# Optimization experiments

Hardware: AMD Instinct MI355X
Metric: run time of the kernel (lower is better)

## Reference

```python
import jax, jax.numpy as jnp
import numpy as np

NUM_HEADS = 16
HEAD_DIM = 64
INNER = NUM_HEADS * HEAD_DIM  # 1024
QUERY_DIM = 1024
CONTEXT_DIM = 768
SCALE = HEAD_DIM ** -0.5


def setup_inputs() -> dict:
    key = jax.random.key(0)
    ks = jax.random.split(key, 6)
    B, NQ, NKV = 8, 1024, 2048
    query = jax.random.normal(ks[0], (B, NQ, QUERY_DIM), dtype=jnp.float32)
    context = jax.random.normal(ks[1], (B, NKV, CONTEXT_DIM), dtype=jnp.float32)
    # weights stored as [in, out] (transpose of torch Linear), math-equivalent
    w_q = jax.random.normal(ks[2], (QUERY_DIM, INNER), dtype=jnp.float32) * (QUERY_DIM ** -0.5)
    w_kv = jax.random.normal(ks[3], (CONTEXT_DIM, 2 * INNER), dtype=jnp.float32) * (CONTEXT_DIM ** -0.5)
    w_out = jax.random.normal(ks[4], (INNER, QUERY_DIM), dtype=jnp.float32) * (INNER ** -0.5)
    b_out = jax.random.normal(ks[5], (QUERY_DIM,), dtype=jnp.float32) * 0.01
    return {"query": query, "context": context, "w_q": w_q, "w_kv": w_kv,
            "w_out": w_out, "b_out": b_out}


def reference(query, context, w_q, w_kv, w_out, b_out):
    B, NQ, _ = query.shape
    NKV = context.shape[1]
    q = query @ w_q                              # [B, NQ, INNER]
    kv = context @ w_kv                          # [B, NKV, 2*INNER]
    k, v = jnp.split(kv, 2, axis=-1)
    # reshape to [B, H, N, D]
    q = q.reshape(B, NQ, NUM_HEADS, HEAD_DIM).transpose(0, 2, 1, 3)
    k = k.reshape(B, NKV, NUM_HEADS, HEAD_DIM).transpose(0, 2, 1, 3)
    v = v.reshape(B, NKV, NUM_HEADS, HEAD_DIM).transpose(0, 2, 1, 3)
    scores = jnp.einsum('bhqd,bhkd->bhqk', q, k) * SCALE
    attn = jax.nn.softmax(scores, axis=-1)
    out = jnp.einsum('bhqk,bhkd->bhqd', attn, v)  # [B, H, NQ, D]
    out = out.transpose(0, 2, 1, 3).reshape(B, NQ, INNER)
    return out @ w_out + b_out
```

## Files before the change

kernel.cpp:

```cpp
#include <hip/hip_runtime.h>
#include <stdint.h>

typedef __bf16 bf16_t;
typedef bf16_t bf16x8 __attribute__((ext_vector_type(8)));
typedef float f32x4 __attribute__((ext_vector_type(4)));
typedef float f32x16 __attribute__((ext_vector_type(16)));

__device__ __forceinline__ unsigned short f2bf(float x) {
    unsigned u = __builtin_bit_cast(unsigned, x);
    u = (u + 0x7FFFu + ((u >> 16) & 1u)) >> 16;
    return (unsigned short)u;
}

__device__ __forceinline__ unsigned pk_bf16(float lo, float hi) {
    unsigned u0 = __builtin_bit_cast(unsigned, lo) + 0x8000u;
    unsigned u1 = __builtin_bit_cast(unsigned, hi) + 0x8000u;
    return __builtin_amdgcn_perm(u1, u0, 0x07060302u);
}

__device__ __forceinline__ void async_load16(const void* g, void* lds) {
    auto* gp = reinterpret_cast<const __attribute__((address_space(1))) uint32_t*>(
        reinterpret_cast<uintptr_t>(g));
    auto* lp = reinterpret_cast<__attribute__((address_space(3))) uint32_t*>(
        reinterpret_cast<uintptr_t>(lds));
    __builtin_amdgcn_global_load_lds(gp, lp, 16, 0, 0);
}

__global__ __launch_bounds__(256) void cast_f32_bf16(const float* __restrict__ src,
                                                     unsigned short* __restrict__ dst,
                                                     int n8) {
    int i = blockIdx.x * 256 + threadIdx.x;
    if (i >= n8) return;
    const float4* s4 = (const float4*)src;
    float4 a = s4[i * 2], b = s4[i * 2 + 1];
    uint4 o;
    o.x = (unsigned)f2bf(a.x) | ((unsigned)f2bf(a.y) << 16);
    o.y = (unsigned)f2bf(a.z) | ((unsigned)f2bf(a.w) << 16);
    o.z = (unsigned)f2bf(b.x) | ((unsigned)f2bf(b.y) << 16);
    o.w = (unsigned)f2bf(b.z) | ((unsigned)f2bf(b.w) << 16);
    ((uint4*)dst)[i] = o;
}

__global__ __launch_bounds__(256) void transcast(const float* __restrict__ src,
                                                 unsigned short* __restrict__ dst,
                                                 int K, int N, float scale) {
    __shared__ float tile[32][33];
    int x = threadIdx.x, y = threadIdx.y;
    int c0 = blockIdx.x * 32, r0 = blockIdx.y * 32;
    #pragma unroll
    for (int i = 0; i < 32; i += 8)
        tile[y + i][x] = src[(size_t)(r0 + y + i) * N + c0 + x];
    __syncthreads();
    #pragma unroll
    for (int i = 0; i < 32; i += 8)
        dst[(size_t)(c0 + y + i) * K + r0 + x] = f2bf(tile[x][y + i] * scale);
}

template <int EPI>
__global__ __launch_bounds__(256) void gemm_bt(const unsigned short* __restrict__ A,
                                               const unsigned short* __restrict__ Bt,
                                               void* __restrict__ Cout,
                                               const float* __restrict__ bias,
                                               int K, int N, int nkt) {
    __shared__ __align__(16) unsigned short lA[128 * 64];
    __shared__ __align__(16) unsigned short lB[128 * 64];
    const int tid = threadIdx.x;
    const int w = tid >> 6, l = tid & 63;
    const int wm = w >> 1, wn = w & 1;
    const int row0 = blockIdx.y * 128, col0 = blockIdx.x * 128;
    const int lrow = l & 15, lq = l >> 4;
    const int srow = l >> 3;
    const int scol = ((l & 7) ^ srow) * 8;

    f32x4 acc[4][4];
    #pragma unroll
    for (int i = 0; i < 4; ++i)
        #pragma unroll
        for (int j = 0; j < 4; ++j) acc[i][j] = (f32x4)0.f;

    for (int kt = 0; kt < nkt; ++kt) {
        const int k0 = kt * 64;
        __syncthreads();
        #pragma unroll
        for (int q = 0; q < 4; ++q) {
            int r = (w * 4 + q) * 8 + srow;
            async_load16(A + (size_t)(row0 + r) * K + k0 + scol,
                         (char*)lA + (w * 4 + q) * 1024);
            async_load16(Bt + (size_t)(col0 + r) * K + k0 + scol,
                         (char*)lB + (w * 4 + q) * 1024);
        }
        __syncthreads();
        #pragma unroll
        for (int kc = 0; kc < 2; ++kc) {
            const int pc = ((kc * 4 + lq) ^ (lrow & 7)) * 16;
            bf16x8 af[4], bfr[4];
            #pragma unroll
            for (int i = 0; i < 4; ++i)
                af[i] = *(const bf16x8*)((const char*)lA + (wm * 64 + i * 16 + lrow) * 128 + pc);
            #pragma unroll
            for (int j = 0; j < 4; ++j)
                bfr[j] = *(const bf16x8*)((const char*)lB + (wn * 64 + j * 16 + lrow) * 128 + pc);
            #pragma unroll
            for (int i = 0; i < 4; ++i)
                #pragma unroll
                for (int j = 0; j < 4; ++j)
                    acc[i][j] = __builtin_amdgcn_mfma_f32_16x16x32_bf16(af[i], bfr[j],
                                                                        acc[i][j], 0, 0, 0);
        }
    }
    #pragma unroll
    for (int i = 0; i < 4; ++i) {
        const int grow0 = row0 + wm * 64 + i * 16 + lq * 4;
        #pragma unroll
        for (int j = 0; j < 4; ++j) {
            const int gcol = col0 + wn * 64 + j * 16 + lrow;
            #pragma unroll
            for (int r = 0; r < 4; ++r) {
                float v = acc[i][j][r];
                int grow = grow0 + r;
                if (EPI == 0) {
                    ((unsigned short*)Cout)[(size_t)grow * N + gcol] = f2bf(v);
                } else {
                    ((float*)Cout)[(size_t)grow * N + gcol] = v + bias[gcol];
                }
            }
        }
    }
}

__global__ __launch_bounds__(256, 2) void gemm_kv(const unsigned short* __restrict__ A,
                                                  const unsigned short* __restrict__ Bt,
                                                  unsigned short* __restrict__ Kb,
                                                  unsigned short* __restrict__ Vt) {
    __shared__ __align__(16) unsigned short lA[256 * 64];
    __shared__ __align__(16) unsigned short lB[128 * 64];
    const int tid = threadIdx.x;
    const int w = tid >> 6, l = tid & 63;
    const int wm = w >> 1, wn = w & 1;
    const int row0 = blockIdx.y * 256, col0 = blockIdx.x * 128;
    const int r32 = l & 31, hw = l >> 5;
    const int srow = l >> 3, scol = ((l & 7) ^ srow) * 8;

    f32x16 acc[4][2];
    #pragma unroll
    for (int mi = 0; mi < 4; ++mi)
        #pragma unroll
        for (int ni = 0; ni < 2; ++ni) acc[mi][ni] = (f32x16)0.f;

    const unsigned short* ga = A + (size_t)(row0 + w * 8 + srow) * 768 + scol;
    const unsigned short* gb = Bt + (size_t)(col0 + w * 8 + srow) * 768 + scol;
    char* lAw = (char*)lA + (w * 8) * 128;
    char* lBw = (char*)lB + (w * 8) * 128;
    const char* lap = (const char*)lA + (wm * 128 + r32) * 128;
    const char* lbp = (const char*)lB + (wn * 64 + r32) * 128;
    const int r7 = r32 & 7;

    for (int kt = 0; kt < 12; ++kt) {
        __syncthreads();
        #pragma unroll
        for (int q = 0; q < 8; ++q)
            async_load16(ga + (size_t)q * 32 * 768, lAw + q * 32 * 128);
        #pragma unroll
        for (int q = 0; q < 4; ++q)
            async_load16(gb + (size_t)q * 32 * 768, lBw + q * 32 * 128);
        ga += 64;
        gb += 64;
        __syncthreads();
        #pragma unroll
        for (int ks = 0; ks < 4; ++ks) {
            const int off = ((ks * 2 + hw) ^ r7) * 16;
            bf16x8 af[4], bfr[2];
            #pragma unroll
            for (int mi = 0; mi < 4; ++mi)
                af[mi] = *(const bf16x8*)(lap + mi * 32 * 128 + off);
            #pragma unroll
            for (int ni = 0; ni < 2; ++ni)
                bfr[ni] = *(const bf16x8*)(lbp + ni * 32 * 128 + off);
            #pragma unroll
            for (int mi = 0; mi < 4; ++mi)
                #pragma unroll
                for (int ni = 0; ni < 2; ++ni)
                    acc[mi][ni] = __builtin_amdgcn_mfma_f32_32x32x16_bf16(af[mi], bfr[ni],
                                                                          acc[mi][ni], 0, 0, 0);
        }
    }

    if (col0 < 1024) {
        unsigned short* kp = Kb + (size_t)(row0 + wm * 128) * 1024 + col0 + wn * 64 + r32;
        #pragma unroll
        for (int mi = 0; mi < 4; ++mi)
            #pragma unroll
            for (int ni = 0; ni < 2; ++ni)
                #pragma unroll
                for (int reg = 0; reg < 16; ++reg) {
                    int rr = mi * 32 + (reg & 3) + 8 * (reg >> 2) + 4 * hw;
                    kp[(size_t)rr * 1024 + ni * 32] = f2bf(acc[mi][ni][reg]);
                }
    } else {
        const int bb = row0 >> 11;
        const int keybase = (row0 & 2047) + wm * 128 + 4 * hw;
        const int fvbase = col0 - 1024 + wn * 64 + r32;
        unsigned short* vp = Vt + ((size_t)bb * 1024 + fvbase) * 2048 + keybase;
        #pragma unroll
        for (int mi = 0; mi < 4; ++mi)
            #pragma unroll
            for (int ni = 0; ni < 2; ++ni)
                #pragma unroll
                for (int g = 0; g < 4; ++g) {
                    uint2 pk2;
                    pk2.x = pk_bf16(acc[mi][ni][g * 4 + 0], acc[mi][ni][g * 4 + 1]);
                    pk2.y = pk_bf16(acc[mi][ni][g * 4 + 2], acc[mi][ni][g * 4 + 3]);
                    *(uint2*)(vp + (size_t)(ni * 32) * 2048 + mi * 32 + g * 8) = pk2;
                }
    }
}

__global__ __launch_bounds__(256, 2) void attn_fwd(const unsigned short* __restrict__ qb,
                                                   const unsigned short* __restrict__ kb,
                                                   const unsigned short* __restrict__ vt,
                                                   unsigned short* __restrict__ ob) {
    constexpr int PSTR = 72;
    __shared__ __align__(16) unsigned short lK[64 * 64];
    __shared__ __align__(16) unsigned short lV[64 * 64];
    __shared__ __align__(16) unsigned short lP[4][32 * PSTR];
    const int tid = threadIdx.x;
    const int w = tid >> 6, l = tid & 63;
    const int bh = blockIdx.x;
    const int b = bh >> 4, h = bh & 15;
    const int q0 = blockIdx.y * 256;
    const int lrow = l & 15, lq = l >> 4;
    const int srow = l >> 3, scol = ((l & 7) ^ (srow & 7)) * 8;

    bf16x8 bq[4][2];
    #pragma unroll
    for (int qs = 0; qs < 4; ++qs)
        #pragma unroll
        for (int kc = 0; kc < 2; ++kc) {
            int row = b * 1024 + q0 + w * 64 + qs * 16 + lrow;
            int col = h * 64 + kc * 32 + lq * 8;
            bq[qs][kc] = *(const bf16x8*)(qb + (size_t)row * 1024 + col);
        }

    f32x4 ot[4][4];
    f32x4 lfr[4];
    #pragma unroll
    for (int qs = 0; qs < 4; ++qs) {
        #pragma unroll
        for (int dt = 0; dt < 4; ++dt) ot[qs][dt] = (f32x4)0.f;
        lfr[qs] = (f32x4)0.f;
    }
    bf16x8 one8;
    #pragma unroll
    for (int i = 0; i < 8; ++i) one8[i] = (bf16_t)1.0f;

    const char* kp0 = (const char*)lK + lrow * 128 + ((lq ^ (lrow & 7)) * 16);
    const char* kp1 = (const char*)lK + lrow * 128 + (((4 + lq) ^ (lrow & 7)) * 16);
    const char* vp0 = (const char*)lV + lrow * 128 + ((lq ^ (lrow & 7)) * 16);
    const char* vp1 = (const char*)lV + lrow * 128 + (((4 + lq) ^ (lrow & 7)) * 16);
    char* pw[2];
    const char* pr[2];
    #pragma unroll
    for (int u = 0; u < 2; ++u) {
        pw[u] = (char*)&lP[w][(u * 16 + lrow) * PSTR + 4 * lq];
        pr[u] = (const char*)&lP[w][(u * 16 + lrow) * PSTR + 8 * lq];
    }

    const unsigned short* gkp = kb + (size_t)b * 2048 * 1024 + h * 64 +
                                (size_t)(w * 8 + srow) * 1024 + scol;
    const unsigned short* gvp = vt + (size_t)(b * 1024 + h * 64) * 2048 +
                                (size_t)(w * 8 + srow) * 2048 + scol;
    char* lKw0 = (char*)lK + (w * 8) * 128;
    char* lKw1 = (char*)lK + (32 + w * 8) * 128;
    char* lVw0 = (char*)lV + (w * 8) * 128;
    char* lVw1 = (char*)lV + (32 + w * 8) * 128;

    for (int it = 0; it < 32; ++it) {
        __syncthreads();
        async_load16(gkp, lKw0);
        async_load16(gkp + 32 * 1024, lKw1);
        async_load16(gvp, lVw0);
        async_load16(gvp + 32 * 2048, lVw1);
        gkp += 64 * 1024;
        gvp += 64;
        __syncthreads();

        bf16x8 ka[4][2], va[4][2];
        #pragma unroll
        for (int mt = 0; mt < 4; ++mt) {
            ka[mt][0] = *(const bf16x8*)(kp0 + mt * 2048);
            ka[mt][1] = *(const bf16x8*)(kp1 + mt * 2048);
        }
        #pragma unroll
        for (int dt = 0; dt < 4; ++dt) {
            va[dt][0] = *(const bf16x8*)(vp0 + dt * 2048);
            va[dt][1] = *(const bf16x8*)(vp1 + dt * 2048);
        }

        #pragma unroll
        for (int p = 0; p < 2; ++p) {
            f32x4 st[2][4];
            #pragma unroll
            for (int u = 0; u < 2; ++u) {
                const int qs = 2 * p + u;
                #pragma unroll
                for (int mt = 0; mt < 4; ++mt) {
                    f32x4 c = (f32x4)0.f;
                    c = __builtin_amdgcn_mfma_f32_16x16x32_bf16(ka[mt][0], bq[qs][0], c, 0, 0, 0);
                    c = __builtin_amdgcn_mfma_f32_16x16x32_bf16(ka[mt][1], bq[qs][1], c, 0, 0, 0);
                    st[u][mt] = c;
                }
            }
            #pragma unroll
            for (int u = 0; u < 2; ++u) {
                #pragma unroll
                for (int mt = 0; mt < 4; ++mt) {
                    #pragma unroll
                    for (int r = 0; r < 4; ++r)
                        st[u][mt][r] = __builtin_amdgcn_exp2f(st[u][mt][r]);
                    uint2 pk;
                    pk.x = pk_bf16(st[u][mt][0], st[u][mt][1]);
                    pk.y = pk_bf16(st[u][mt][2], st[u][mt][3]);
                    *(uint2*)(pw[u] + 32 * mt) = pk;
                }
            }
            bf16x8 pb[2][2];
            #pragma unroll
            for (int u = 0; u < 2; ++u)
                #pragma unroll
                for (int kcg = 0; kcg < 2; ++kcg)
                    pb[u][kcg] = *(const bf16x8*)(pr[u] + 64 * kcg);
            #pragma unroll
            for (int u = 0; u < 2; ++u) {
                const int qs = 2 * p + u;
                lfr[qs] = __builtin_amdgcn_mfma_f32_16x16x32_bf16(one8, pb[u][0], lfr[qs], 0, 0, 0);
                lfr[qs] = __builtin_amdgcn_mfma_f32_16x16x32_bf16(one8, pb[u][1], lfr[qs], 0, 0, 0);
                #pragma unroll
                for (int dt = 0; dt < 4; ++dt) {
                    ot[qs][dt] = __builtin_amdgcn_mfma_f32_16x16x32_bf16(va[dt][0], pb[u][0], ot[qs][dt], 0, 0, 0);
                    ot[qs][dt] = __builtin_amdgcn_mfma_f32_16x16x32_bf16(va[dt][1], pb[u][1], ot[qs][dt], 0, 0, 0);
                }
            }
        }
    }

    #pragma unroll
    for (int qs = 0; qs < 4; ++qs) {
        float inv = 1.f / lfr[qs][0];
        size_t grow = (size_t)(b * 1024 + q0 + w * 64 + qs * 16 + lrow);
        unsigned short* op = ob + grow * 1024 + h * 64 + 4 * lq;
        #pragma unroll
        for (int dt = 0; dt < 4; ++dt) {
            uint2 pk;
            pk.x = pk_bf16(ot[qs][dt][0] * inv, ot[qs][dt][1] * inv);
            pk.y = pk_bf16(ot[qs][dt][2] * inv, ot[qs][dt][3] * inv);
            *(uint2*)(op + 16 * dt) = pk;
        }
    }
}

extern "C" void kernel_launch(void* const* d_in, const int* in_sizes, int n_in,
                              void* d_out, int out_size, void* d_ws, size_t ws_size,
                              hipStream_t stream) {
    const float* query   = (const float*)d_in[0];
    const float* context = (const float*)d_in[1];
    const float* w_q     = (const float*)d_in[2];
    const float* w_kv    = (const float*)d_in[3];
    const float* w_out   = (const float*)d_in[4];
    const float* b_out   = (const float*)d_in[5];
    float* out = (float*)d_out;

    char* p = (char*)d_ws;
    unsigned short* qin   = (unsigned short*)p; p += (size_t)8192 * 1024 * 2;
    unsigned short* cin   = (unsigned short*)p; p += (size_t)16384 * 768 * 2;
    unsigned short* wqT   = (unsigned short*)p; p += (size_t)1024 * 1024 * 2;
    unsigned short* wkvT  = (unsigned short*)p; p += (size_t)2048 * 768 * 2;
    unsigned short* woutT = (unsigned short*)p; p += (size_t)1024 * 1024 * 2;
    unsigned short* qproj = (unsigned short*)p; p += (size_t)8192 * 1024 * 2;
    unsigned short* kbuf  = (unsigned short*)p; p += (size_t)16384 * 1024 * 2;
    unsigned short* vT    = (unsigned short*)p; p += (size_t)16384 * 1024 * 2;
    unsigned short* obuf  = (unsigned short*)p; p += (size_t)8192 * 1024 * 2;

    const float qscale = 0.125f * 1.44269504088896f;

    cast_f32_bf16<<<8388608 / 8 / 256, 256, 0, stream>>>(query, qin, 8388608 / 8);
    cast_f32_bf16<<<12582912 / 8 / 256, 256, 0, stream>>>(context, cin, 12582912 / 8);
    transcast<<<dim3(32, 32), dim3(32, 8), 0, stream>>>(w_q, wqT, 1024, 1024, qscale);
    transcast<<<dim3(64, 24), dim3(32, 8), 0, stream>>>(w_kv, wkvT, 768, 2048, 1.0f);
    transcast<<<dim3(32, 32), dim3(32, 8), 0, stream>>>(w_out, woutT, 1024, 1024, 1.0f);
    gemm_bt<0><<<dim3(8, 64), 256, 0, stream>>>(qin, wqT, qproj, nullptr, 1024, 1024, 16);
    gemm_kv<<<dim3(16, 64), 256, 0, stream>>>(cin, wkvT, kbuf, vT);
    attn_fwd<<<dim3(128, 4), 256, 0, stream>>>(qproj, kbuf, vT, obuf);
    gemm_bt<2><<<dim3(8, 64), 256, 0, stream>>>(obuf, woutT, out, b_out, 1024, 1024, 16);
}
```

Baseline: 349.8 us.

## Double-buffer LDS tiles in GEMM and attention, add MFMA wave priority hints

Both the bf16 GEMM and the attention kernel now keep two LDS buffers. The next K/V (or A/B) tile is issued as an async global-to-LDS load before computing on the current one, leaving one barrier per iteration instead of two. This is meant to hide global load latency behind MFMA work. The attention kernel also raises wave priority around its MFMA blocks with s_setprio. The cost is doubled LDS use per block, which could limit occupancy, and the overlap relies on the barrier waiting for the outstanding async loads.

```diff
diff --git a/kernel.cpp b/kernel.cpp
--- a/kernel.cpp
+++ b/kernel.cpp
@@ -62,8 +62,8 @@
                                                void* __restrict__ Cout,
                                                const float* __restrict__ bias,
                                                int K, int N, int nkt) {
-    __shared__ __align__(16) unsigned short lA[128 * 64];
-    __shared__ __align__(16) unsigned short lB[128 * 64];
+    __shared__ __align__(16) unsigned short lA[2][128 * 64];
+    __shared__ __align__(16) unsigned short lB[2][128 * 64];
     const int tid = threadIdx.x;
     const int w = tid >> 6, l = tid & 63;
     const int wm = w >> 1, wn = w & 1;
@@ -78,28 +78,46 @@
         #pragma unroll
         for (int j = 0; j < 4; ++j) acc[i][j] = (f32x4)0.f;
 
+    const unsigned short* ga[4];
+    const unsigned short* gb[4];
+    #pragma unroll
+    for (int q = 0; q < 4; ++q) {
+        const int r = (w * 4 + q) * 8 + srow;
+        ga[q] = A + (size_t)(row0 + r) * K + scol;
+        gb[q] = Bt + (size_t)(col0 + r) * K + scol;
+    }
+
+    #pragma unroll
+    for (int q = 0; q < 4; ++q) {
+        async_load16(ga[q], (char*)lA + (w * 4 + q) * 1024);
+        async_load16(gb[q], (char*)lB + (w * 4 + q) * 1024);
+        ga[q] += 64;
+        gb[q] += 64;
+    }
+    __syncthreads();
+
     for (int kt = 0; kt < nkt; ++kt) {
-        const int k0 = kt * 64;
-        __syncthreads();
-        #pragma unroll
-        for (int q = 0; q < 4; ++q) {
-            int r = (w * 4 + q) * 8 + srow;
-            async_load16(A + (size_t)(row0 + r) * K + k0 + scol,
-                         (char*)lA + (w * 4 + q) * 1024);
-            async_load16(Bt + (size_t)(col0 + r) * K + k0 + scol,
-                         (char*)lB + (w * 4 + q) * 1024);
-        }
-        __syncthreads();
+        const int bo = (kt & 1) * 16384;
+        if (kt + 1 < nkt) {
+            const int bn = bo ^ 16384;
+            #pragma unroll
+            for (int q = 0; q < 4; ++q) {
+                async_load16(ga[q], (char*)lA + bn + (w * 4 + q) * 1024);
+                async_load16(gb[q], (char*)lB + bn + (w * 4 + q) * 1024);
+                ga[q] += 64;
+                gb[q] += 64;
+            }
+        }
         #pragma unroll
         for (int kc = 0; kc < 2; ++kc) {
             const int pc = ((kc * 4 + lq) ^ (lrow & 7)) * 16;
             bf16x8 af[4], bfr[4];
             #pragma unroll
             for (int i = 0; i < 4; ++i)
-                af[i] = *(const bf16x8*)((const char*)lA + (wm * 64 + i * 16 + lrow) * 128 + pc);
+                af[i] = *(const bf16x8*)((const char*)lA + bo + (wm * 64 + i * 16 + lrow) * 128 + pc);
             #pragma unroll
             for (int j = 0; j < 4; ++j)
-                bfr[j] = *(const bf16x8*)((const char*)lB + (wn * 64 + j * 16 + lrow) * 128 + pc);
+                bfr[j] = *(const bf16x8*)((const char*)lB + bo + (wn * 64 + j * 16 + lrow) * 128 + pc);
             #pragma unroll
             for (int i = 0; i < 4; ++i)
                 #pragma unroll
@@ -107,6 +125,7 @@
                     acc[i][j] = __builtin_amdgcn_mfma_f32_16x16x32_bf16(af[i], bfr[j],
                                                                         acc[i][j], 0, 0, 0);
         }
+        __syncthreads();
     }
     #pragma unroll
     for (int i = 0; i < 4; ++i) {
@@ -220,8 +239,8 @@
                                                    const unsigned short* __restrict__ vt,
                                                    unsigned short* __restrict__ ob) {
     constexpr int PSTR = 72;
-    __shared__ __align__(16) unsigned short lK[64 * 64];
-    __shared__ __align__(16) unsigned short lV[64 * 64];
+    __shared__ __align__(16) unsigned short lK[2][64 * 64];
+    __shared__ __align__(16) unsigned short lV[2][64 * 64];
     __shared__ __align__(16) unsigned short lP[4][32 * PSTR];
     const int tid = threadIdx.x;
     const int w = tid >> 6, l = tid & 63;
@@ -274,31 +293,42 @@
     char* lVw0 = (char*)lV + (w * 8) * 128;
     char* lVw1 = (char*)lV + (32 + w * 8) * 128;
 
+    async_load16(gkp, lKw0);
+    async_load16(gkp + 32 * 1024, lKw1);
+    async_load16(gvp, lVw0);
+    async_load16(gvp + 32 * 2048, lVw1);
+    gkp += 64 * 1024;
+    gvp += 64;
+    __syncthreads();
+
     for (int it = 0; it < 32; ++it) {
-        __syncthreads();
-        async_load16(gkp, lKw0);
-        async_load16(gkp + 32 * 1024, lKw1);
-        async_load16(gvp, lVw0);
-        async_load16(gvp + 32 * 2048, lVw1);
-        gkp += 64 * 1024;
-        gvp += 64;
-        __syncthreads();
+        const int bo = (it & 1) * 8192;
+        if (it < 31) {
+            const int bn = bo ^ 8192;
+            async_load16(gkp, lKw0 + bn);
+            async_load16(gkp + 32 * 1024, lKw1 + bn);
+            async_load16(gvp, lVw0 + bn);
+            async_load16(gvp + 32 * 2048, lVw1 + bn);
+            gkp += 64 * 1024;
+            gvp += 64;
+        }
 
         bf16x8 ka[4][2], va[4][2];
         #pragma unroll
         for (int mt = 0; mt < 4; ++mt) {
-            ka[mt][0] = *(const bf16x8*)(kp0 + mt * 2048);
-            ka[mt][1] = *(const bf16x8*)(kp1 + mt * 2048);
+            ka[mt][0] = *(const bf16x8*)(kp0 + bo + mt * 2048);
+            ka[mt][1] = *(const bf16x8*)(kp1 + bo + mt * 2048);
         }
         #pragma unroll
         for (int dt = 0; dt < 4; ++dt) {
-            va[dt][0] = *(const bf16x8*)(vp0 + dt * 2048);
-            va[dt][1] = *(const bf16x8*)(vp1 + dt * 2048);
+            va[dt][0] = *(const bf16x8*)(vp0 + bo + dt * 2048);
+            va[dt][1] = *(const bf16x8*)(vp1 + bo + dt * 2048);
         }
 
         #pragma unroll
         for (int p = 0; p < 2; ++p) {
             f32x4 st[2][4];
+            __builtin_amdgcn_s_setprio(1);
             #pragma unroll
             for (int u = 0; u < 2; ++u) {
                 const int qs = 2 * p + u;
@@ -310,6 +340,7 @@
                     st[u][mt] = c;
                 }
             }
+            __builtin_amdgcn_s_setprio(0);
             #pragma unroll
             for (int u = 0; u < 2; ++u) {
                 #pragma unroll
@@ -329,6 +360,7 @@
                 #pragma unroll
                 for (int kcg = 0; kcg < 2; ++kcg)
                     pb[u][kcg] = *(const bf16x8*)(pr[u] + 64 * kcg);
+            __builtin_amdgcn_s_setprio(1);
             #pragma unroll
             for (int u = 0; u < 2; ++u) {
                 const int qs = 2 * p + u;
@@ -340,7 +372,9 @@
                     ot[qs][dt] = __builtin_amdgcn_mfma_f32_16x16x32_bf16(va[dt][1], pb[u][1], ot[qs][dt], 0, 0, 0);
                 }
             }
-        }
+            __builtin_amdgcn_s_setprio(0);
+        }
+        __syncthreads();
     }
 
     #pragma unroll
```

New measurement: 340.4 us. 1.03x faster.
